# Kernel optimization log

Measured on AMD Instinct MI355X. Metric: run time of the kernel, lower is better.

## Reference

```python
import jax, jax.numpy as jnp
import numpy as np

N_SEQ, N_RES, C_M = 512, 384, 256
C_O, C_Z = 32, 128  # num_outer_channel, num_output_channel
LN_EPS = 1e-5
NORM_EPS = 1e-3


def setup_inputs() -> dict:
    key = jax.random.key(0)
    ks = jax.random.split(key, 8)
    scale = 1.0 / np.sqrt(C_M)
    return {
        "act": jax.random.normal(ks[0], (N_SEQ, N_RES, C_M), dtype=jnp.float32),
        "mask": jax.random.uniform(ks[1], (N_SEQ, N_RES), dtype=jnp.float32),
        "ln_w": jnp.ones((C_M,), dtype=jnp.float32),
        "ln_b": jnp.zeros((C_M,), dtype=jnp.float32),
        "left_w": jax.random.normal(ks[2], (C_O, C_M), dtype=jnp.float32) * scale,
        "left_b": jnp.zeros((C_O,), dtype=jnp.float32),
        "right_w": jax.random.normal(ks[3], (C_O, C_M), dtype=jnp.float32) * scale,
        "right_b": jnp.zeros((C_O,), dtype=jnp.float32),
        "output_w": jax.random.normal(ks[4], (C_O, C_O, C_Z), dtype=jnp.float32) * (1.0 / C_O),
        "output_b": jnp.zeros((C_Z,), dtype=jnp.float32),
    }


def reference(act, mask, ln_w, ln_b, left_w, left_b, right_w, right_b, output_w, output_b):
    # LayerNorm over c_m
    mu = jnp.mean(act, axis=-1, keepdims=True)
    var = jnp.var(act, axis=-1, keepdims=True)
    act_n = (act - mu) * jax.lax.rsqrt(var + LN_EPS) * ln_w + ln_b

    m = mask[..., None]  # [s, r, 1]
    left = m * (jnp.einsum("src,oc->sro", act_n, left_w) + left_b)    # [s, r, co]
    right = m * (jnp.einsum("src,oc->sro", act_n, right_w) + right_b)  # [s, r, co]

    # outer product over sequence dim, then contract with output_w:
    # out[b, d, f] = sum_{a, c, e} left[a, b, c] * right[a, d, e] * w[c, e, f]
    outer = jnp.einsum("abc,ade->bdce", left, right)          # [r, r, co, co]
    out = jnp.einsum("bdce,cef->bdf", outer, output_w) + output_b  # [r, r, c_z]

    norm = jnp.einsum("sb,sd->bd", mask, mask)[..., None]  # [r, r, 1]
    return out / (NORM_EPS + norm)
```

## Files before the change

### kernel.cpp

```cpp
#include <hip/hip_runtime.h>

typedef short short8 __attribute__((ext_vector_type(8)));
typedef short short4v __attribute__((ext_vector_type(4)));
typedef float f32x4 __attribute__((ext_vector_type(4)));
typedef unsigned short ushort_t;

#define DEV_INLINE __device__ __forceinline__

constexpr int NSEQ = 512, NRES = 384, CM = 256, CO = 32, CZ = 128;
constexpr float F_LN_EPS = 1e-5f, F_NORM_EPS = 1e-3f;

constexpr size_t WS_LT   = 0;
constexpr size_t WS_RT   = WS_LT + (size_t)12288 * 512 * 2;
constexpr size_t WS_WT   = WS_RT + (size_t)12288 * 512 * 2;
constexpr size_t WS_NORM = WS_WT + (size_t)128 * 1024 * 2;
constexpr size_t WS_PW   = WS_NORM + (size_t)384 * 384 * 4;

DEV_INLINE ushort_t f2bf(float x) {
  union { float f; unsigned u; } v; v.f = x;
  unsigned r = v.u + 0x7FFFu + ((v.u >> 16) & 1u);
  return (ushort_t)(r >> 16);
}

DEV_INLINE short8 pack8(float4 a, float4 b) {
  short8 p;
  p[0] = (short)f2bf(a.x); p[1] = (short)f2bf(a.y);
  p[2] = (short)f2bf(a.z); p[3] = (short)f2bf(a.w);
  p[4] = (short)f2bf(b.x); p[5] = (short)f2bf(b.y);
  p[6] = (short)f2bf(b.z); p[7] = (short)f2bf(b.w);
  return p;
}

DEV_INLINE void async16(const void* g, void* l) {
  __builtin_amdgcn_global_load_lds(
      (const __attribute__((address_space(1))) unsigned*)g,
      (__attribute__((address_space(3))) unsigned*)l, 16, 0, 0);
}

__global__ __launch_bounds__(256) void k_wt(const float* __restrict__ W,
                                            ushort_t* __restrict__ WT) {
  int tid = blockIdx.x * 256 + threadIdx.x;
  int f = tid >> 10, ce = tid & 1023;
  WT[tid] = f2bf(W[(size_t)ce * CZ + f]);
}

__global__ __launch_bounds__(256) void k_pack(const float* __restrict__ left_w,
                                              const float* __restrict__ right_w,
                                              ushort_t* __restrict__ PW) {
  int id = blockIdx.x * 256 + threadIdx.x;
  int o = id >> 5, ch = id & 31;
  const float* src = (o < 32 ? left_w + (size_t)o * CM
                             : right_w + (size_t)(o - 32) * CM) + ch * 8;
  float4 a = *(const float4*)src, b = *(const float4*)(src + 4);
  *(short8*)&PW[(size_t)o * CM + ch * 8] = pack8(a, b);
}

__global__ __launch_bounds__(256) void k_norm(const float* __restrict__ mask,
                                              float* __restrict__ normM) {
  int b = blockIdx.x * 16 + threadIdx.x;
  int d = blockIdx.y * 16 + threadIdx.y;
  float a0 = 0.f, a1 = 0.f, a2 = 0.f, a3 = 0.f;
  for (int a = 0; a < NSEQ; a += 4) {
    a0 += mask[(size_t)(a + 0) * NRES + b] * mask[(size_t)(a + 0) * NRES + d];
    a1 += mask[(size_t)(a + 1) * NRES + b] * mask[(size_t)(a + 1) * NRES + d];
    a2 += mask[(size_t)(a + 2) * NRES + b] * mask[(size_t)(a + 2) * NRES + d];
    a3 += mask[(size_t)(a + 3) * NRES + b] * mask[(size_t)(a + 3) * NRES + d];
  }
  normM[(size_t)b * NRES + d] = (a0 + a1) + (a2 + a3);
}

__global__ __launch_bounds__(256) void k_lnproj(
    const float* __restrict__ act, const float* __restrict__ mask,
    const float* __restrict__ ln_w, const float* __restrict__ ln_b,
    const float* __restrict__ left_b, const float* __restrict__ right_b,
    const ushort_t* __restrict__ PW,
    ushort_t* __restrict__ Lt, ushort_t* __restrict__ Rt) {
  __shared__ ushort_t sAct[16 * 256];

  const int t = threadIdx.x;
  const int a0 = blockIdx.x * 16;
  const int b = blockIdx.y;
  const int r = t >> 4, c = t & 15;

  const float4* arow =
      (const float4*)(act + ((size_t)(a0 + r) * NRES + b) * CM + c * 16);
  float4 v[4];
  float s = 0.f, ss = 0.f;
#pragma unroll
  for (int j = 0; j < 4; j++) {
    v[j] = arow[j];
    s += v[j].x + v[j].y + v[j].z + v[j].w;
    ss += v[j].x * v[j].x + v[j].y * v[j].y + v[j].z * v[j].z + v[j].w * v[j].w;
  }
  s += __shfl_xor(s, 1);  s += __shfl_xor(s, 2);
  s += __shfl_xor(s, 4);  s += __shfl_xor(s, 8);
  ss += __shfl_xor(ss, 1); ss += __shfl_xor(ss, 2);
  ss += __shfl_xor(ss, 4); ss += __shfl_xor(ss, 8);
  const float mu = s * (1.f / CM);
  const float rs = rsqrtf(ss * (1.f / CM) - mu * mu + F_LN_EPS);

  const int lane = t & 63, w = t >> 6;
  const int q = lane >> 4, ln = lane & 15;
  short8 bfrag[8];
#pragma unroll
  for (int ks = 0; ks < 8; ks++)
    bfrag[ks] = *(const short8*)&PW[(size_t)(w * 16 + ln) * CM + (ks * 4 + q) * 8];

#pragma unroll
  for (int j = 0; j < 2; j++) {
    int cb = c * 16 + j * 8;
    float4 lw0 = *(const float4*)(ln_w + cb), lw1 = *(const float4*)(ln_w + cb + 4);
    float4 lb0 = *(const float4*)(ln_b + cb), lb1 = *(const float4*)(ln_b + cb + 4);
    float4 x0 = v[2 * j], x1 = v[2 * j + 1], y0, y1;
    y0.x = (x0.x - mu) * rs * lw0.x + lb0.x;
    y0.y = (x0.y - mu) * rs * lw0.y + lb0.y;
    y0.z = (x0.z - mu) * rs * lw0.z + lb0.z;
    y0.w = (x0.w - mu) * rs * lw0.w + lb0.w;
    y1.x = (x1.x - mu) * rs * lw1.x + lb1.x;
    y1.y = (x1.y - mu) * rs * lw1.y + lb1.y;
    y1.z = (x1.z - mu) * rs * lw1.z + lb1.z;
    y1.w = (x1.w - mu) * rs * lw1.w + lb1.w;
    int chunk = c * 2 + j;
    *(short8*)&sAct[r * 256 + ((chunk ^ (r & 7)) * 8)] = pack8(y0, y1);
  }
  __syncthreads();

  f32x4 acc = {0, 0, 0, 0};
#pragma unroll
  for (int ks = 0; ks < 8; ks++) {
    int kc = ks * 4 + q;
    short8 af = *(const short8*)&sAct[ln * 256 + ((kc ^ (ln & 7)) * 8)];
    acc = __builtin_amdgcn_mfma_f32_16x16x32_bf16(af, bfrag[ks], acc, 0, 0, 0);
  }

  const int o = w * 16 + ln;
  float mk[4];
#pragma unroll
  for (int reg = 0; reg < 4; reg++)
    mk[reg] = mask[(size_t)(a0 + q * 4 + reg) * NRES + b];
  float bias = (o < 32) ? left_b[o] : right_b[o - 32];
  ushort_t* dst = (o < 32) ? (Lt + (size_t)(b * 32 + o) * NSEQ)
                           : (Rt + (size_t)(b * 32 + (o - 32)) * NSEQ);
  short4v pk;
#pragma unroll
  for (int reg = 0; reg < 4; reg++)
    pk[reg] = (short)f2bf((acc[reg] + bias) * mk[reg]);
  *(short4v*)&dst[a0 + q * 4] = pk;
}

__global__ __launch_bounds__(256, 3) void k_opm(
    const ushort_t* __restrict__ Lt, const ushort_t* __restrict__ Rt,
    const ushort_t* __restrict__ WT, const float* __restrict__ normM,
    const float* __restrict__ out_b, float* __restrict__ out) {
  __shared__ ushort_t smem[24576];
  ushort_t* sA = smem;
  ushort_t* sB = smem + 8192;
  ushort_t* sP = smem;
  ushort_t* sW = smem + 16384;

  const int t = threadIdx.x, lane = t & 63, w = t >> 6;
  const int q = lane >> 4, ln = lane & 15;
  const int wm = w & 1, wn = w >> 1;
  const int m0 = blockIdx.x * 128, n0 = blockIdx.y * 128;
  const int srow8 = lane >> 3, schunk = lane & 7;

  f32x4 acc1[4][4];
#pragma unroll
  for (int i = 0; i < 4; i++)
#pragma unroll
    for (int j = 0; j < 4; j++) acc1[i][j] = {0, 0, 0, 0};

  for (int kt = 0; kt < 8; kt++) {
    __syncthreads();
#pragma unroll
    for (int i = 0; i < 4; i++) {
      int rg = w + i * 4;
      int r = rg * 8 + srow8;
      int gc = schunk ^ (r & 7);
      async16(Lt + (size_t)(m0 + r) * NSEQ + kt * 64 + gc * 8, (char*)sA + rg * 1024);
      async16(Rt + (size_t)(n0 + r) * NSEQ + kt * 64 + gc * 8, (char*)sB + rg * 1024);
    }
    __syncthreads();
#pragma unroll
    for (int ks = 0; ks < 2; ks++) {
      int kc = ks * 4 + q;
      short8 af[4], bf[4];
#pragma unroll
      for (int tm = 0; tm < 4; tm++) {
        int rr = wm * 64 + tm * 16 + ln;
        af[tm] = *(const short8*)&sA[rr * 64 + ((kc ^ (rr & 7)) * 8)];
      }
#pragma unroll
      for (int tn = 0; tn < 4; tn++) {
        int rr = wn * 64 + tn * 16 + ln;
        bf[tn] = *(const short8*)&sB[rr * 64 + ((kc ^ (rr & 7)) * 8)];
      }
#pragma unroll
      for (int tm = 0; tm < 4; tm++)
#pragma unroll
        for (int tn = 0; tn < 4; tn++)
          acc1[tm][tn] =
              __builtin_amdgcn_mfma_f32_16x16x32_bf16(af[tm], bf[tn], acc1[tm][tn], 0, 0, 0);
    }
  }

  __syncthreads();
#pragma unroll
  for (int tm = 0; tm < 4; tm++) {
#pragma unroll
    for (int tn = 0; tn < 4; tn++) {
      int pair = (wm * 2 + (tm >> 1)) * 4 + (wn * 2 + (tn >> 1));
      int e = (tn & 1) * 16 + ln;
#pragma unroll
      for (int reg = 0; reg < 4; reg++) {
        int c = (tm & 1) * 16 + q * 4 + reg;
        int ce = c * 32 + e;
        int pos = (ce >> 3) ^ (pair & 7);
        sP[pair * 1024 + pos * 8 + (ce & 7)] = f2bf(acc1[tm][tn][reg]);
      }
    }
  }
  __syncthreads();

  f32x4 acc2[2] = {{0, 0, 0, 0}, {0, 0, 0, 0}};
  for (int kt = 0; kt < 16; kt++) {
    if (kt) __syncthreads();
#pragma unroll
    for (int i = 0; i < 4; i++) {
      int rg = w + i * 4;
      int r = rg * 8 + srow8;
      int gc = schunk ^ (r & 7);
      async16(WT + (size_t)r * 1024 + kt * 64 + gc * 8, (char*)sW + rg * 1024);
    }
    __syncthreads();
#pragma unroll
    for (int ks = 0; ks < 2; ks++) {
      int pchunk = kt * 8 + ks * 4 + q;
      short8 af = *(const short8*)&sP[ln * 1024 + ((pchunk ^ (ln & 7)) * 8)];
      int kc = ks * 4 + q;
#pragma unroll
      for (int tn = 0; tn < 2; tn++) {
        int fr = w * 32 + tn * 16 + ln;
        short8 bf = *(const short8*)&sW[fr * 64 + ((kc ^ (fr & 7)) * 8)];
        acc2[tn] = __builtin_amdgcn_mfma_f32_16x16x32_bf16(af, bf, acc2[tn], 0, 0, 0);
      }
    }
  }

  const int b = blockIdx.x * 4 + q;
#pragma unroll
  for (int reg = 0; reg < 4; reg++) {
    int d = blockIdx.y * 4 + reg;
    float inv = 1.f / (F_NORM_EPS + normM[(size_t)b * NRES + d]);
#pragma unroll
    for (int tn = 0; tn < 2; tn++) {
      int f = w * 32 + tn * 16 + ln;
      out[((size_t)b * NRES + d) * CZ + f] = (acc2[tn][reg] + out_b[f]) * inv;
    }
  }
}

extern "C" void kernel_launch(void* const* d_in, const int* in_sizes, int n_in,
                              void* d_out, int out_size, void* d_ws, size_t ws_size,
                              hipStream_t stream) {
  (void)in_sizes; (void)n_in; (void)out_size; (void)ws_size;
  const float* act      = (const float*)d_in[0];
  const float* mask     = (const float*)d_in[1];
  const float* ln_w     = (const float*)d_in[2];
  const float* ln_b     = (const float*)d_in[3];
  const float* left_w   = (const float*)d_in[4];
  const float* left_b   = (const float*)d_in[5];
  const float* right_w  = (const float*)d_in[6];
  const float* right_b  = (const float*)d_in[7];
  const float* output_w = (const float*)d_in[8];
  const float* output_b = (const float*)d_in[9];
  float* out = (float*)d_out;

  char* ws = (char*)d_ws;
  ushort_t* Lt = (ushort_t*)(ws + WS_LT);
  ushort_t* Rt = (ushort_t*)(ws + WS_RT);
  ushort_t* WT = (ushort_t*)(ws + WS_WT);
  float* normM = (float*)(ws + WS_NORM);
  ushort_t* PW = (ushort_t*)(ws + WS_PW);

  hipLaunchKernelGGL(k_pack, dim3(8), dim3(256), 0, stream, left_w, right_w, PW);
  hipLaunchKernelGGL(k_wt, dim3(512), dim3(256), 0, stream, output_w, WT);
  hipLaunchKernelGGL(k_norm, dim3(24, 24), dim3(16, 16), 0, stream, mask, normM);
  hipLaunchKernelGGL(k_lnproj, dim3(32, 384), dim3(256), 0, stream, act, mask,
                     ln_w, ln_b, left_b, right_b, PW, Lt, Rt);
  hipLaunchKernelGGL(k_opm, dim3(96, 96), dim3(256), 0, stream, Lt, Rt, WT,
                     normM, output_b, out);
}
```

Measured before the change: 627.9 us.

## Double-buffer stage-1 LDS loads and read output weights directly from global

The first GEMM in k_opm now double-buffers the Lt/Rt tiles in LDS, issuing the next k-tile's async loads before computing on the current one, and raises MFMA wave priority with s_setprio. The second GEMM no longer stages output weights through LDS. The weights are re-laid out in k_wt so each lane can load its 8-element fragment straight from global/L2. This removes per-iteration barriers and LDS staging, at the cost of doubling LDS (64KB), lowering the occupancy hint from 3 to 2 blocks, and adding global-memory latency in the second GEMM.

```diff
diff --git a/kernel.cpp b/kernel.cpp
--- a/kernel.cpp
+++ b/kernel.cpp
@@ -38,10 +38,10 @@
 }
 
 __global__ __launch_bounds__(256) void k_wt(const float* __restrict__ W,
-                                            ushort_t* __restrict__ WT) {
+                                            ushort_t* __restrict__ WT2) {
   int tid = blockIdx.x * 256 + threadIdx.x;
-  int f = tid >> 10, ce = tid & 1023;
-  WT[tid] = f2bf(W[(size_t)ce * CZ + f]);
+  int k = tid >> 7, f = tid & 127;
+  WT2[((size_t)(k >> 3) * 128 + f) * 8 + (k & 7)] = f2bf(W[(size_t)k * CZ + f]);
 }
 
 __global__ __launch_bounds__(256) void k_pack(const float* __restrict__ left_w,
@@ -148,15 +148,12 @@
   *(short4v*)&dst[a0 + q * 4] = pk;
 }
 
-__global__ __launch_bounds__(256, 3) void k_opm(
+__global__ __launch_bounds__(256, 2) void k_opm(
     const ushort_t* __restrict__ Lt, const ushort_t* __restrict__ Rt,
-    const ushort_t* __restrict__ WT, const float* __restrict__ normM,
+    const ushort_t* __restrict__ WT2, const float* __restrict__ normM,
     const float* __restrict__ out_b, float* __restrict__ out) {
-  __shared__ ushort_t smem[24576];
-  ushort_t* sA = smem;
-  ushort_t* sB = smem + 8192;
+  __shared__ ushort_t smem[32768];
   ushort_t* sP = smem;
-  ushort_t* sW = smem + 16384;
 
   const int t = threadIdx.x, lane = t & 63, w = t >> 6;
   const int q = lane >> 4, ln = lane & 15;
@@ -164,23 +161,35 @@
   const int m0 = blockIdx.x * 128, n0 = blockIdx.y * 128;
   const int srow8 = lane >> 3, schunk = lane & 7;
 
-  f32x4 acc1[4][4];
-#pragma unroll
-  for (int i = 0; i < 4; i++)
-#pragma unroll
-    for (int j = 0; j < 4; j++) acc1[i][j] = {0, 0, 0, 0};
-
-  for (int kt = 0; kt < 8; kt++) {
-    __syncthreads();
+  auto STAGE = [&](int kt, int c) {
+    ushort_t* base = smem + c * 16384;
 #pragma unroll
     for (int i = 0; i < 4; i++) {
       int rg = w + i * 4;
       int r = rg * 8 + srow8;
       int gc = schunk ^ (r & 7);
-      async16(Lt + (size_t)(m0 + r) * NSEQ + kt * 64 + gc * 8, (char*)sA + rg * 1024);
-      async16(Rt + (size_t)(n0 + r) * NSEQ + kt * 64 + gc * 8, (char*)sB + rg * 1024);
-    }
-    __syncthreads();
+      async16(Lt + (size_t)(m0 + r) * NSEQ + kt * 64 + gc * 8, (char*)base + rg * 1024);
+      async16(Rt + (size_t)(n0 + r) * NSEQ + kt * 64 + gc * 8,
+              (char*)base + 16384 + rg * 1024);
+    }
+  };
+
+  f32x4 acc1[4][4];
+#pragma unroll
+  for (int i = 0; i < 4; i++)
+#pragma unroll
+    for (int j = 0; j < 4; j++) acc1[i][j] = {0, 0, 0, 0};
+
+  STAGE(0, 0);
+  asm volatile("s_waitcnt vmcnt(0)" ::: "memory");
+  __builtin_amdgcn_s_barrier();
+#pragma unroll
+  for (int kt = 0; kt < 8; kt++) {
+    const int cur = kt & 1;
+    if (kt + 1 < 8) STAGE(kt + 1, cur ^ 1);
+
+    const ushort_t* bA = smem + cur * 16384;
+    const ushort_t* bB = bA + 8192;
 #pragma unroll
     for (int ks = 0; ks < 2; ks++) {
       int kc = ks * 4 + q;
@@ -188,20 +197,24 @@
 #pragma unroll
       for (int tm = 0; tm < 4; tm++) {
         int rr = wm * 64 + tm * 16 + ln;
-        af[tm] = *(const short8*)&sA[rr * 64 + ((kc ^ (rr & 7)) * 8)];
+        af[tm] = *(const short8*)&bA[rr * 64 + ((kc ^ (rr & 7)) * 8)];
       }
 #pragma unroll
       for (int tn = 0; tn < 4; tn++) {
         int rr = wn * 64 + tn * 16 + ln;
-        bf[tn] = *(const short8*)&sB[rr * 64 + ((kc ^ (rr & 7)) * 8)];
-      }
+        bf[tn] = *(const short8*)&bB[rr * 64 + ((kc ^ (rr & 7)) * 8)];
+      }
+      __builtin_amdgcn_s_setprio(1);
 #pragma unroll
       for (int tm = 0; tm < 4; tm++)
 #pragma unroll
         for (int tn = 0; tn < 4; tn++)
           acc1[tm][tn] =
               __builtin_amdgcn_mfma_f32_16x16x32_bf16(af[tm], bf[tn], acc1[tm][tn], 0, 0, 0);
-    }
+      __builtin_amdgcn_s_setprio(0);
+    }
+    asm volatile("s_waitcnt vmcnt(0)" ::: "memory");
+    __builtin_amdgcn_s_barrier();
   }
 
   __syncthreads();
@@ -223,26 +236,17 @@
   __syncthreads();
 
   f32x4 acc2[2] = {{0, 0, 0, 0}, {0, 0, 0, 0}};
+#pragma unroll
   for (int kt = 0; kt < 16; kt++) {
-    if (kt) __syncthreads();
-#pragma unroll
-    for (int i = 0; i < 4; i++) {
-      int rg = w + i * 4;
-      int r = rg * 8 + srow8;
-      int gc = schunk ^ (r & 7);
-      async16(WT + (size_t)r * 1024 + kt * 64 + gc * 8, (char*)sW + rg * 1024);
-    }
-    __syncthreads();
 #pragma unroll
     for (int ks = 0; ks < 2; ks++) {
-      int pchunk = kt * 8 + ks * 4 + q;
-      short8 af = *(const short8*)&sP[ln * 1024 + ((pchunk ^ (ln & 7)) * 8)];
-      int kc = ks * 4 + q;
+      int c16 = kt * 8 + ks * 4 + q;
+      short8 af = *(const short8*)&sP[ln * 1024 + ((c16 ^ (ln & 7)) * 8)];
 #pragma unroll
       for (int tn = 0; tn < 2; tn++) {
         int fr = w * 32 + tn * 16 + ln;
-        short8 bf = *(const short8*)&sW[fr * 64 + ((kc ^ (fr & 7)) * 8)];
-        acc2[tn] = __builtin_amdgcn_mfma_f32_16x16x32_bf16(af, bf, acc2[tn], 0, 0, 0);
+        short8 bfr = *(const short8*)&WT2[((size_t)c16 * 128 + fr) * 8];
+        acc2[tn] = __builtin_amdgcn_mfma_f32_16x16x32_bf16(af, bfr, acc2[tn], 0, 0, 0);
       }
     }
   }
@@ -279,15 +283,15 @@
   char* ws = (char*)d_ws;
   ushort_t* Lt = (ushort_t*)(ws + WS_LT);
   ushort_t* Rt = (ushort_t*)(ws + WS_RT);
-  ushort_t* WT = (ushort_t*)(ws + WS_WT);
+  ushort_t* WT2 = (ushort_t*)(ws + WS_WT);
   float* normM = (float*)(ws + WS_NORM);
   ushort_t* PW = (ushort_t*)(ws + WS_PW);
 
   hipLaunchKernelGGL(k_pack, dim3(8), dim3(256), 0, stream, left_w, right_w, PW);
-  hipLaunchKernelGGL(k_wt, dim3(512), dim3(256), 0, stream, output_w, WT);
+  hipLaunchKernelGGL(k_wt, dim3(512), dim3(256), 0, stream, output_w, WT2);
   hipLaunchKernelGGL(k_norm, dim3(24, 24), dim3(16, 16), 0, stream, mask, normM);
   hipLaunchKernelGGL(k_lnproj, dim3(32, 384), dim3(256), 0, stream, act, mask,
                      ln_w, ln_b, left_b, right_b, PW, Lt, Rt);
-  hipLaunchKernelGGL(k_opm, dim3(96, 96), dim3(256), 0, stream, Lt, Rt, WT,
+  hipLaunchKernelGGL(k_opm, dim3(96, 96), dim3(256), 0, stream, Lt, Rt, WT2,
                      normM, output_b, out);
 }
```

Result: faster. 590.6 us (-5.9%).
